# Kernel optimization log

Measured on AMD Instinct MI355X. Metric: run time of the kernel, lower is better.

## Reference

```python
import jax, jax.numpy as jnp
import numpy as np

N, E = 100000, 1000000
IN_F, HID, OUT, K = 64, 64, 32, 3


def setup_inputs() -> dict:
    key = jax.random.key(0)
    ks = jax.random.split(key, 8)
    s = 0.05
    return {
        "features": jax.random.normal(ks[0], (N, IN_F), dtype=jnp.float32),
        "src": jax.random.randint(ks[1], (E,), 0, N),
        "dst": jax.random.randint(ks[2], (E,), 0, N),
        "n_nodes": N,
        "W1": jax.random.normal(ks[3], (K * IN_F, HID), jnp.float32) * s,
        "b1": jnp.zeros((HID,), jnp.float32),
        "W2": jax.random.normal(ks[4], (K * HID, HID), jnp.float32) * s,
        "b2": jnp.zeros((HID,), jnp.float32),
        "Wm1": jax.random.normal(ks[5], (HID, HID), jnp.float32) * s,
        "bm1": jnp.zeros((HID,), jnp.float32),
        "Wm2": jax.random.normal(ks[6], (HID, OUT), jnp.float32) * s,
        "bm2": jnp.zeros((OUT,), jnp.float32),
    }


def _cheb_conv(x, src, dst, dinv, W, b, n_nodes, k=K):
    # DGL ChebConv with lambda_max = 2 (re_norm = 2/lambda_max = 1).
    def prop(h):  # D^{-1/2} A D^{-1/2} h via edge gather/scatter
        m = (h * dinv)[src]                                   # [E, F]
        agg = jax.ops.segment_sum(m, dst, num_segments=n_nodes)
        return agg * dinv

    X0 = x
    Xs = [X0]
    X1 = -prop(X0)                 # -re_norm*L h + (re_norm-1)*X0, re_norm=1
    Xs.append(X1)
    for _ in range(2, k):
        Xi = -2.0 * prop(X1) - X0  # Chebyshev recursion
        Xs.append(Xi)
        X0, X1 = X1, Xi
    return jnp.concatenate(Xs, axis=1) @ W + b  # Linear(k*F_in -> F_out)


def reference(features, src, dst, n_nodes, W1, b1, W2, b2, Wm1, bm1, Wm2, bm2):
    deg = jax.ops.segment_sum(
        jnp.ones((src.shape[0],), dtype=features.dtype), dst, num_segments=n_nodes
    )
    dinv = (jnp.clip(deg, 1.0, None) ** -0.5)[:, None]  # in-degree^{-1/2}
    x = jax.nn.relu(_cheb_conv(features, src, dst, dinv, W1, b1, n_nodes))
    x = jax.nn.relu(_cheb_conv(x, src, dst, dinv, W2, b2, n_nodes))
    return jax.nn.relu(x @ Wm1 + bm1) @ Wm2 + bm2
```

## Files before the change

### kernel.cpp

```cpp
#include <hip/hip_runtime.h>


typedef unsigned short ushort_t;
typedef __attribute__((ext_vector_type(8))) short v8s;
typedef __attribute__((ext_vector_type(4))) float v4f;

__device__ inline ushort_t f2bf(float f) {
    unsigned u = __float_as_uint(f);
    return (ushort_t)((u + 0x7FFFu + ((u >> 16) & 1u)) >> 16);
}
__device__ inline float bf2f(ushort_t h) {
    return __uint_as_float(((unsigned)h) << 16);
}

#define BSH 9
#define BSZ (1 << BSH)
#define CHUNK 4096

__global__ void k_wprep(const float* __restrict__ W1, const float* __restrict__ W2,
                        const float* __restrict__ Wm1, const float* __restrict__ Wm2,
                        ushort_t* __restrict__ W1t, ushort_t* __restrict__ W2t,
                        ushort_t* __restrict__ Wm1t, ushort_t* __restrict__ Wm2t,
                        int* __restrict__ gbase, int* __restrict__ done, int NB) {
    int i = blockIdx.x * 256 + threadIdx.x;
    if (i < 12288) { int k = i >> 6, n = i & 63; W1t[n * 192 + k] = f2bf(W1[i]); return; }
    i -= 12288;
    if (i < 12288) { int k = i >> 6, n = i & 63; W2t[n * 192 + k] = f2bf(W2[i]); return; }
    i -= 12288;
    if (i < 4096) { int k = i >> 6, n = i & 63; Wm1t[n * 64 + k] = f2bf(Wm1[i]); return; }
    i -= 4096;
    if (i < 2048) { int k = i >> 5, n = i & 31; Wm2t[n * 64 + k] = f2bf(Wm2[i]); return; }
    i -= 2048;
    if (i < NB) gbase[i] = 0;
    if (i == NB) *done = 0;
}

__global__ __launch_bounds__(256) void k_bhist(const int* __restrict__ dst,
                                               int* __restrict__ gbase,
                                               int* __restrict__ gcur,
                                               int* __restrict__ done, int E, int NB) {
    __shared__ int h[1024];
    __shared__ int isLast;
    for (int i = threadIdx.x; i < NB; i += 256) h[i] = 0;
    __syncthreads();
    for (int i = blockIdx.x * blockDim.x + threadIdx.x; i < E; i += gridDim.x * blockDim.x)
        atomicAdd(&h[dst[i] >> BSH], 1);
    __syncthreads();
    for (int i = threadIdx.x; i < NB; i += 256)
        if (h[i]) atomicAdd(&gbase[i], h[i]);
    __threadfence();
    __syncthreads();
    if (threadIdx.x == 0) isLast = (atomicAdd(done, 1) == (int)gridDim.x - 1);
    __syncthreads();
    if (isLast) {
        __threadfence();
        int t = threadIdx.x;
        int v = (t < NB) ? gbase[t] : 0;
        h[t] = v;
        __syncthreads();
        for (int off = 1; off < 256; off <<= 1) {
            int u = (t >= off) ? h[t - off] : 0;
            __syncthreads();
            h[t] += u;
            __syncthreads();
        }
        if (t < NB) {
            int excl = h[t] - v;
            gbase[t] = excl;
            gcur[t] = excl;
        }
    }
}

__global__ __launch_bounds__(256) void k_bucket2(
    const int* __restrict__ src, const int* __restrict__ dst,
    int* __restrict__ gcur, int2* __restrict__ eb, int E, int NB) {
    __shared__ int ls[CHUNK];
    __shared__ int ld[CHUNK];
    __shared__ int hist[1024];
    __shared__ int bbase[1024];
    int t = threadIdx.x;
    int base = blockIdx.x * CHUNK;
    int count = E - base;
    if (count > CHUNK) count = CHUNK;
    for (int i = t; i < NB; i += 256) hist[i] = 0;
    __syncthreads();
    for (int i = t; i < count; i += 256) {
        int s = src[base + i];
        int d = dst[base + i];
        ls[i] = s;
        ld[i] = d;
        atomicAdd(&hist[d >> BSH], 1);
    }
    __syncthreads();
    for (int b = t; b < NB; b += 256) {
        int c = hist[b];
        bbase[b] = c ? atomicAdd(&gcur[b], c) : 0;
        hist[b] = 0;
    }
    __syncthreads();
    for (int i = t; i < count; i += 256) {
        int d = ld[i];
        int b = d >> BSH;
        int off = atomicAdd(&hist[b], 1);
        eb[bbase[b] + off] = make_int2(ls[i], d);
    }
}

__global__ __launch_bounds__(256) void k_local(
    const int2* __restrict__ eb, const int* __restrict__ gbase,
    int* __restrict__ col, int* __restrict__ row_ptr,
    float* __restrict__ dinv, int N, int E, int NB) {
    __shared__ int cnt[BSZ];
    __shared__ int tsum[256];
    int t = threadIdx.x;
    int b = blockIdx.x;
    int d0 = b << BSH;
    cnt[2 * t] = 0;
    cnt[2 * t + 1] = 0;
    __syncthreads();
    int beg = gbase[b];
    int end = (b + 1 < NB) ? gbase[b + 1] : E;
    for (int i = beg + t; i < end; i += 256)
        atomicAdd(&cnt[eb[i].y - d0], 1);
    __syncthreads();
    int c0 = cnt[2 * t], c1 = cnt[2 * t + 1];
    int mysum = c0 + c1;
    tsum[t] = mysum;
    __syncthreads();
    for (int off = 1; off < 256; off <<= 1) {
        int u = 0;
        if (t >= off) u = tsum[t - off];
        __syncthreads();
        tsum[t] += u;
        __syncthreads();
    }
    int rbase = beg + tsum[t] - mysum;
    int d = d0 + 2 * t;
    if (d < N) {
        row_ptr[d] = rbase;
        dinv[d] = rsqrtf(fmaxf((float)c0, 1.0f));
    }
    if (d + 1 < N) {
        row_ptr[d + 1] = rbase + c0;
        dinv[d + 1] = rsqrtf(fmaxf((float)c1, 1.0f));
    }
    cnt[2 * t] = rbase;
    cnt[2 * t + 1] = rbase + c0;
    __syncthreads();
    for (int i = beg + t; i < end; i += 256) {
        int2 e = eb[i];
        int p = atomicAdd(&cnt[e.y - d0], 1);
        col[p] = e.x;
    }
    if (b == NB - 1 && t == 0) row_ptr[N] = E;
}

__global__ void k_tobf16(const float4* __restrict__ X, const float* __restrict__ dinv,
                         ushort4* __restrict__ Y, int n4) {
    int i = blockIdx.x * blockDim.x + threadIdx.x;
    if (i < n4) {
        float s = dinv[i >> 4];
        float4 v = X[i];
        ushort4 o;
        o.x = f2bf(v.x * s); o.y = f2bf(v.y * s); o.z = f2bf(v.z * s); o.w = f2bf(v.w * s);
        Y[i] = o;
    }
}

template <int MODE>
__global__ __launch_bounds__(256) void k_prop(
    const ushort_t* __restrict__ Xb, const int* __restrict__ rp,
    const int* __restrict__ col, const float* __restrict__ dinv,
    const ushort_t* __restrict__ X0b, ushort_t* __restrict__ OUTB, int N) {
    int wid = (blockIdx.x * blockDim.x + threadIdx.x) >> 6;
    int lane = threadIdx.x & 63;
    if (wid >= N) return;
    int g = lane >> 4;
    int fl = (lane & 15) * 4;
    int beg = rp[wid], end = rp[wid + 1];
    float4 a0 = make_float4(0.f, 0.f, 0.f, 0.f);
    float4 a1 = make_float4(0.f, 0.f, 0.f, 0.f);
    int e = beg + g;
    for (; e + 4 < end; e += 8) {
        int s0 = col[e], s1 = col[e + 4];
        ushort4 u0 = *(const ushort4*)&Xb[(size_t)s0 * 64 + fl];
        ushort4 u1 = *(const ushort4*)&Xb[(size_t)s1 * 64 + fl];
        a0.x += bf2f(u0.x); a0.y += bf2f(u0.y); a0.z += bf2f(u0.z); a0.w += bf2f(u0.w);
        a1.x += bf2f(u1.x); a1.y += bf2f(u1.y); a1.z += bf2f(u1.z); a1.w += bf2f(u1.w);
    }
    if (e < end) {
        int s0 = col[e];
        ushort4 u0 = *(const ushort4*)&Xb[(size_t)s0 * 64 + fl];
        a0.x += bf2f(u0.x); a0.y += bf2f(u0.y); a0.z += bf2f(u0.z); a0.w += bf2f(u0.w);
    }
    float4 acc;
    acc.x = a0.x + a1.x;
    acc.y = a0.y + a1.y;
    acc.z = a0.z + a1.z;
    acc.w = a0.w + a1.w;
    acc.x += __shfl_xor(acc.x, 16);
    acc.y += __shfl_xor(acc.y, 16);
    acc.z += __shfl_xor(acc.z, 16);
    acc.w += __shfl_xor(acc.w, 16);
    acc.x += __shfl_xor(acc.x, 32);
    acc.y += __shfl_xor(acc.y, 32);
    acc.z += __shfl_xor(acc.z, 32);
    acc.w += __shfl_xor(acc.w, 32);
    if (g == 0) {
        float di = dinv[wid];
        ushort4 ob;
        if (MODE == 1) {
            float m = -di * di;
            ob.x = f2bf(m * acc.x);
            ob.y = f2bf(m * acc.y);
            ob.z = f2bf(m * acc.z);
            ob.w = f2bf(m * acc.w);
        } else {
            ushort4 x0u = *(const ushort4*)&X0b[(size_t)wid * 64 + fl];
            float m = -2.0f * di;
            float rd = 1.0f / di;
            ob.x = f2bf(fmaf(m, acc.x, -rd * bf2f(x0u.x)));
            ob.y = f2bf(fmaf(m, acc.y, -rd * bf2f(x0u.y)));
            ob.z = f2bf(fmaf(m, acc.z, -rd * bf2f(x0u.z)));
            ob.w = f2bf(fmaf(m, acc.w, -rd * bf2f(x0u.w)));
        }
        *(ushort4*)&OUTB[(size_t)wid * 64 + fl] = ob;
    }
}

template <bool SCALE_OUT>
__global__ __launch_bounds__(256, 4) void k_cheb_mfma(
    const ushort_t* __restrict__ X0, const ushort_t* __restrict__ X1,
    const ushort_t* __restrict__ X2, const float* __restrict__ dinv,
    const ushort_t* __restrict__ Wt, const float* __restrict__ b,
    ushort_t* __restrict__ Yb, int N) {
    __shared__ ushort_t XA[3][64][72];
    int tid = threadIdx.x;
    int node0 = blockIdx.x * 64;
    const ushort_t* Xc[3] = {X0, X1, X2};
#pragma unroll
    for (int c = 0; c < 3; c++) {
#pragma unroll
        for (int p = 0; p < 2; p++) {
            int s = p * 2048 + tid * 8;
            int row = s >> 6, cc = s & 63;
            v8s v = *(const v8s*)&Xc[c][((size_t)(node0 + row)) * 64 + cc];
            *(v8s*)&XA[c][row][cc] = v;
        }
    }
    __syncthreads();

    int wave = tid >> 6, lane = tid & 63;
    int n16 = lane & 15, q = lane >> 4;
    int lrow = wave * 16 + n16;
    v8s av[6];
#pragma unroll
    for (int ks = 0; ks < 6; ks++)
        av[ks] = *(const v8s*)&XA[ks >> 1][lrow][(ks & 1) * 32 + q * 8];

    v4f acc_s[4], acc_u[4];
#pragma unroll
    for (int t = 0; t < 4; t++) {
        acc_s[t] = (v4f){0.f, 0.f, 0.f, 0.f};
        acc_u[t] = (v4f){0.f, 0.f, 0.f, 0.f};
    }
#pragma unroll
    for (int ks = 0; ks < 6; ks++) {
        int c = ks >> 1;
#pragma unroll
        for (int t = 0; t < 4; t++) {
            v8s bv = *(const v8s*)&Wt[(size_t)(t * 16 + n16) * 192 + ks * 32 + q * 8];
            if (c < 2)
                acc_s[t] = __builtin_amdgcn_mfma_f32_16x16x32_bf16(av[ks], bv, acc_s[t], 0, 0, 0);
            else
                acc_u[t] = __builtin_amdgcn_mfma_f32_16x16x32_bf16(av[ks], bv, acc_u[t], 0, 0, 0);
        }
    }
    int rbase = node0 + wave * 16 + q * 4;
#pragma unroll
    for (int r = 0; r < 4; r++) {
        int row = rbase + r;
        if (row < N) {
            float dv = dinv[row];
            float rd = 1.0f / dv;
            float s = SCALE_OUT ? dv : 1.0f;
#pragma unroll
            for (int t = 0; t < 4; t++) {
                float y = fmaf(rd, acc_s[t][r], acc_u[t][r]) + b[t * 16 + n16];
                y = fmaxf(y, 0.0f);
                Yb[(size_t)row * 64 + t * 16 + n16] = f2bf(s * y);
            }
        }
    }
}

__global__ __launch_bounds__(256, 4) void k_cheb_mlp(
    const ushort_t* __restrict__ X0, const ushort_t* __restrict__ X1,
    const ushort_t* __restrict__ X2, const float* __restrict__ dinv,
    const ushort_t* __restrict__ Wt, const float* __restrict__ b,
    const ushort_t* __restrict__ Wm1t, const float* __restrict__ bm1,
    const ushort_t* __restrict__ Wm2t, const float* __restrict__ bm2,
    float* __restrict__ out, int N) {
    __shared__ ushort_t smem[3 * 64 * 72];
    ushort_t (*XA)[64][72] = (ushort_t(*)[64][72])smem;
    ushort_t (*Hs0)[76] = (ushort_t(*)[76])smem;
    ushort_t (*Hs1)[76] = (ushort_t(*)[76])(smem + 64 * 76);
    int tid = threadIdx.x;
    int node0 = blockIdx.x * 64;
    const ushort_t* Xc[3] = {X0, X1, X2};
#pragma unroll
    for (int c = 0; c < 3; c++) {
#pragma unroll
        for (int p = 0; p < 2; p++) {
            int s = p * 2048 + tid * 8;
            int row = s >> 6, cc = s & 63;
            v8s v = *(const v8s*)&Xc[c][((size_t)(node0 + row)) * 64 + cc];
            *(v8s*)&XA[c][row][cc] = v;
        }
    }
    __syncthreads();

    int wave = tid >> 6, lane = tid & 63;
    int n16 = lane & 15, q = lane >> 4;
    int lrow = wave * 16 + n16;
    v8s av[6];
#pragma unroll
    for (int ks = 0; ks < 6; ks++)
        av[ks] = *(const v8s*)&XA[ks >> 1][lrow][(ks & 1) * 32 + q * 8];
    __syncthreads();

    v4f acc_s[4], acc_u[4];
#pragma unroll
    for (int t = 0; t < 4; t++) {
        acc_s[t] = (v4f){0.f, 0.f, 0.f, 0.f};
        acc_u[t] = (v4f){0.f, 0.f, 0.f, 0.f};
    }
#pragma unroll
    for (int ks = 0; ks < 6; ks++) {
        int c = ks >> 1;
#pragma unroll
        for (int t = 0; t < 4; t++) {
            v8s bv = *(const v8s*)&Wt[(size_t)(t * 16 + n16) * 192 + ks * 32 + q * 8];
            if (c < 2)
                acc_s[t] = __builtin_amdgcn_mfma_f32_16x16x32_bf16(av[ks], bv, acc_s[t], 0, 0, 0);
            else
                acc_u[t] = __builtin_amdgcn_mfma_f32_16x16x32_bf16(av[ks], bv, acc_u[t], 0, 0, 0);
        }
    }
    int lr = wave * 16 + q * 4;
    int rbase = node0 + lr;
#pragma unroll
    for (int r = 0; r < 4; r++) {
        int row = rbase + r;
        if (row < N) {
            float dv = dinv[row];
            float rd = 1.0f / dv;
#pragma unroll
            for (int t = 0; t < 4; t++) {
                float y = fmaf(rd, acc_s[t][r], acc_u[t][r]) + b[t * 16 + n16];
                Hs0[lr + r][t * 16 + n16] = f2bf(fmaxf(y, 0.0f));
            }
        } else {
#pragma unroll
            for (int t = 0; t < 4; t++) Hs0[lr + r][t * 16 + n16] = 0;
        }
    }
    __syncthreads();

    v4f acc[4];
#pragma unroll
    for (int t = 0; t < 4; t++) acc[t] = (v4f){0.f, 0.f, 0.f, 0.f};
#pragma unroll
    for (int ks = 0; ks < 2; ks++) {
        v8s av1 = *(const v8s*)&Hs0[wave * 16 + n16][ks * 32 + q * 8];
#pragma unroll
        for (int t = 0; t < 4; t++) {
            v8s bv = *(const v8s*)&Wm1t[(size_t)(t * 16 + n16) * 64 + ks * 32 + q * 8];
            acc[t] = __builtin_amdgcn_mfma_f32_16x16x32_bf16(av1, bv, acc[t], 0, 0, 0);
        }
    }
#pragma unroll
    for (int r = 0; r < 4; r++)
#pragma unroll
        for (int t = 0; t < 4; t++) {
            float y = acc[t][r] + bm1[t * 16 + n16];
            Hs1[lr + r][t * 16 + n16] = f2bf(fmaxf(y, 0.0f));
        }
    __syncthreads();

    v4f a2[2];
    a2[0] = (v4f){0.f, 0.f, 0.f, 0.f};
    a2[1] = (v4f){0.f, 0.f, 0.f, 0.f};
#pragma unroll
    for (int ks = 0; ks < 2; ks++) {
        v8s av2 = *(const v8s*)&Hs1[wave * 16 + n16][ks * 32 + q * 8];
#pragma unroll
        for (int t = 0; t < 2; t++) {
            v8s bv = *(const v8s*)&Wm2t[(size_t)(t * 16 + n16) * 64 + ks * 32 + q * 8];
            a2[t] = __builtin_amdgcn_mfma_f32_16x16x32_bf16(av2, bv, a2[t], 0, 0, 0);
        }
    }
#pragma unroll
    for (int r = 0; r < 4; r++) {
        int row = rbase + r;
        if (row < N) {
#pragma unroll
            for (int t = 0; t < 2; t++)
                out[(size_t)row * 32 + t * 16 + n16] = a2[t][r] + bm2[t * 16 + n16];
        }
    }
}

extern "C" void kernel_launch(void* const* d_in, const int* in_sizes, int n_in,
                              void* d_out, int out_size, void* d_ws, size_t ws_size,
                              hipStream_t stream) {
    const float* features = (const float*)d_in[0];
    const int* src = (const int*)d_in[1];
    const int* dst = (const int*)d_in[2];
    const float* W1 = (const float*)d_in[4];
    const float* b1 = (const float*)d_in[5];
    const float* W2 = (const float*)d_in[6];
    const float* b2 = (const float*)d_in[7];
    const float* Wm1 = (const float*)d_in[8];
    const float* bm1 = (const float*)d_in[9];
    const float* Wm2 = (const float*)d_in[10];
    const float* bm2 = (const float*)d_in[11];
    float* out = (float*)d_out;

    int N = in_sizes[0] / 64;
    int E = in_sizes[1];
    int NB = (N + BSZ - 1) >> BSH;

    float* ws = (float*)d_ws;
    float* dinv = ws;
    int* row_ptr = (int*)(dinv + N);
    int* gbase = row_ptr + (N + 1);
    int* gcur = gbase + 1024;
    int* done = gcur + 1024;
    int* col = done + 16;
    int2* eb = (int2*)(((uintptr_t)(col + E) + 7) & ~(uintptr_t)7);
    ushort_t* Fb  = (ushort_t*)(eb + E);
    ushort_t* X1b = Fb  + (size_t)N * 64;
    ushort_t* X2b = X1b + (size_t)N * 64;
    ushort_t* H1b = X2b + (size_t)N * 64;
    ushort_t* W1t = H1b + (size_t)N * 64;
    ushort_t* W2t = W1t + 64 * 192;
    ushort_t* Wm1t = W2t + 64 * 192;
    ushort_t* Wm2t = Wm1t + 64 * 64;

    int pblk = (N * 64 + 255) / 256;
    int gblk = (N + 63) / 64;
    int n4 = N * 16;
    int cblk = (n4 + 255) / 256;
    int bblk = (E + CHUNK - 1) / CHUNK;

    k_wprep<<<(30720 + 1024 + 255) / 256, 256, 0, stream>>>(
        W1, W2, Wm1, Wm2, W1t, W2t, Wm1t, Wm2t, gbase, done, NB);

    k_bhist<<<512, 256, 0, stream>>>(dst, gbase, gcur, done, E, NB);
    k_bucket2<<<bblk, 256, 0, stream>>>(src, dst, gcur, eb, E, NB);
    k_local<<<NB, 256, 0, stream>>>(eb, gbase, col, row_ptr, dinv, N, E, NB);

    k_tobf16<<<cblk, 256, 0, stream>>>((const float4*)features, dinv, (ushort4*)Fb, n4);

    k_prop<1><<<pblk, 256, 0, stream>>>(Fb, row_ptr, col, dinv, nullptr, X1b, N);
    k_prop<2><<<pblk, 256, 0, stream>>>(X1b, row_ptr, col, dinv, Fb, X2b, N);
    k_cheb_mfma<true><<<gblk, 256, 0, stream>>>(Fb, X1b, X2b, dinv, W1t, b1, H1b, N);

    k_prop<1><<<pblk, 256, 0, stream>>>(H1b, row_ptr, col, dinv, nullptr, X1b, N);
    k_prop<2><<<pblk, 256, 0, stream>>>(X1b, row_ptr, col, dinv, H1b, X2b, N);
    k_cheb_mlp<<<gblk, 256, 0, stream>>>(H1b, X1b, X2b, dinv, W2t, b2,
                                         Wm1t, bm1, Wm2t, bm2, out, N);
}
```

Before: 402.5 us.

## Fuse second Chebyshev propagation into the MFMA linear kernels

```diff
diff --git a/kernel.cpp b/kernel.cpp
--- a/kernel.cpp
+++ b/kernel.cpp
@@ -166,6 +166,34 @@
         o.x = f2bf(v.x * s); o.y = f2bf(v.y * s); o.z = f2bf(v.z * s); o.w = f2bf(v.w * s);
         Y[i] = o;
     }
+}
+
+__device__ inline float4 gather_sum(const ushort_t* __restrict__ Xb,
+                                    const int* __restrict__ col,
+                                    int beg, int end, int g, int fl) {
+    float4 a0 = make_float4(0.f, 0.f, 0.f, 0.f);
+    float4 a1 = make_float4(0.f, 0.f, 0.f, 0.f);
+    int e = beg + g;
+    for (; e + 4 < end; e += 8) {
+        int s0 = col[e], s1 = col[e + 4];
+        ushort4 u0 = *(const ushort4*)&Xb[(size_t)s0 * 64 + fl];
+        ushort4 u1 = *(const ushort4*)&Xb[(size_t)s1 * 64 + fl];
+        a0.x += bf2f(u0.x); a0.y += bf2f(u0.y); a0.z += bf2f(u0.z); a0.w += bf2f(u0.w);
+        a1.x += bf2f(u1.x); a1.y += bf2f(u1.y); a1.z += bf2f(u1.z); a1.w += bf2f(u1.w);
+    }
+    if (e < end) {
+        int s0 = col[e];
+        ushort4 u0 = *(const ushort4*)&Xb[(size_t)s0 * 64 + fl];
+        a0.x += bf2f(u0.x); a0.y += bf2f(u0.y); a0.z += bf2f(u0.z); a0.w += bf2f(u0.w);
+    }
+    float4 acc;
+    acc.x = a0.x + a1.x; acc.y = a0.y + a1.y;
+    acc.z = a0.z + a1.z; acc.w = a0.w + a1.w;
+    acc.x += __shfl_xor(acc.x, 16); acc.y += __shfl_xor(acc.y, 16);
+    acc.z += __shfl_xor(acc.z, 16); acc.w += __shfl_xor(acc.w, 16);
+    acc.x += __shfl_xor(acc.x, 32); acc.y += __shfl_xor(acc.y, 32);
+    acc.z += __shfl_xor(acc.z, 32); acc.w += __shfl_xor(acc.w, 32);
+    return acc;
 }
 
 template <int MODE>
@@ -229,126 +257,160 @@
     }
 }
 
-template <bool SCALE_OUT>
-__global__ __launch_bounds__(256, 4) void k_cheb_mfma(
-    const ushort_t* __restrict__ X0, const ushort_t* __restrict__ X1,
-    const ushort_t* __restrict__ X2, const float* __restrict__ dinv,
-    const ushort_t* __restrict__ Wt, const float* __restrict__ b,
-    ushort_t* __restrict__ Yb, int N) {
-    __shared__ ushort_t XA[3][64][72];
+__global__ __launch_bounds__(512, 8) void k_pc1(
+    const ushort_t* __restrict__ Xb, const int* __restrict__ rp,
+    const int* __restrict__ col, const float* __restrict__ dinv,
+    const ushort_t* __restrict__ T0, const ushort_t* __restrict__ Wt,
+    const float* __restrict__ b, ushort_t* __restrict__ Yb, int N) {
+    __shared__ ushort_t XA[64][72];
     int tid = threadIdx.x;
+    int w = tid >> 6, lane = tid & 63;
+    int g = lane >> 4, fl = (lane & 15) * 4;
     int node0 = blockIdx.x * 64;
-    const ushort_t* Xc[3] = {X0, X1, X2};
-#pragma unroll
-    for (int c = 0; c < 3; c++) {
-#pragma unroll
-        for (int p = 0; p < 2; p++) {
-            int s = p * 2048 + tid * 8;
-            int row = s >> 6, cc = s & 63;
-            v8s v = *(const v8s*)&Xc[c][((size_t)(node0 + row)) * 64 + cc];
-            *(v8s*)&XA[c][row][cc] = v;
-        }
-    }
-    __syncthreads();
-
-    int wave = tid >> 6, lane = tid & 63;
+
+    for (int i = 0; i < 8; i++) {
+        int nd = node0 + w * 8 + i;
+        ushort4 ob;
+        ob.x = 0; ob.y = 0; ob.z = 0; ob.w = 0;
+        if (nd < N) {
+            float4 acc = gather_sum(Xb, col, rp[nd], rp[nd + 1], g, fl);
+            if (g == 0) {
+                float di = dinv[nd];
+                ushort4 x0u = *(const ushort4*)&T0[(size_t)nd * 64 + fl];
+                float m = -2.0f * di;
+                float rd = 1.0f / di;
+                ob.x = f2bf(fmaf(m, acc.x, -rd * bf2f(x0u.x)));
+                ob.y = f2bf(fmaf(m, acc.y, -rd * bf2f(x0u.y)));
+                ob.z = f2bf(fmaf(m, acc.z, -rd * bf2f(x0u.z)));
+                ob.w = f2bf(fmaf(m, acc.w, -rd * bf2f(x0u.w)));
+            }
+        }
+        if (g == 0) *(ushort4*)&XA[w * 8 + i][fl] = ob;
+    }
+    __syncthreads();
+
     int n16 = lane & 15, q = lane >> 4;
-    int lrow = wave * 16 + n16;
-    v8s av[6];
-#pragma unroll
-    for (int ks = 0; ks < 6; ks++)
-        av[ks] = *(const v8s*)&XA[ks >> 1][lrow][(ks & 1) * 32 + q * 8];
-
-    v4f acc_s[4], acc_u[4];
-#pragma unroll
-    for (int t = 0; t < 4; t++) {
-        acc_s[t] = (v4f){0.f, 0.f, 0.f, 0.f};
-        acc_u[t] = (v4f){0.f, 0.f, 0.f, 0.f};
-    }
+    int f = w >> 1, h = w & 1;
+    int arow = node0 + f * 16 + n16;
+
+    v4f acc_s[2], acc_u[2];
+    acc_s[0] = (v4f){0.f, 0.f, 0.f, 0.f};
+    acc_s[1] = (v4f){0.f, 0.f, 0.f, 0.f};
+    acc_u[0] = (v4f){0.f, 0.f, 0.f, 0.f};
+    acc_u[1] = (v4f){0.f, 0.f, 0.f, 0.f};
 #pragma unroll
     for (int ks = 0; ks < 6; ks++) {
         int c = ks >> 1;
-#pragma unroll
-        for (int t = 0; t < 4; t++) {
+        int kk = (ks & 1) * 32 + q * 8;
+        v8s av = {0, 0, 0, 0, 0, 0, 0, 0};
+        if (c == 2) {
+            av = *(const v8s*)&XA[f * 16 + n16][kk];
+        } else {
+            const ushort_t* P = (c == 0) ? T0 : Xb;
+            if (arow < N) av = *(const v8s*)&P[(size_t)arow * 64 + kk];
+        }
+#pragma unroll
+        for (int t2 = 0; t2 < 2; t2++) {
+            int t = h * 2 + t2;
             v8s bv = *(const v8s*)&Wt[(size_t)(t * 16 + n16) * 192 + ks * 32 + q * 8];
             if (c < 2)
-                acc_s[t] = __builtin_amdgcn_mfma_f32_16x16x32_bf16(av[ks], bv, acc_s[t], 0, 0, 0);
+                acc_s[t2] = __builtin_amdgcn_mfma_f32_16x16x32_bf16(av, bv, acc_s[t2], 0, 0, 0);
             else
-                acc_u[t] = __builtin_amdgcn_mfma_f32_16x16x32_bf16(av[ks], bv, acc_u[t], 0, 0, 0);
-        }
-    }
-    int rbase = node0 + wave * 16 + q * 4;
+                acc_u[t2] = __builtin_amdgcn_mfma_f32_16x16x32_bf16(av, bv, acc_u[t2], 0, 0, 0);
+        }
+    }
+    int rbase = node0 + f * 16 + q * 4;
 #pragma unroll
     for (int r = 0; r < 4; r++) {
         int row = rbase + r;
         if (row < N) {
             float dv = dinv[row];
             float rd = 1.0f / dv;
-            float s = SCALE_OUT ? dv : 1.0f;
-#pragma unroll
-            for (int t = 0; t < 4; t++) {
-                float y = fmaf(rd, acc_s[t][r], acc_u[t][r]) + b[t * 16 + n16];
+#pragma unroll
+            for (int t2 = 0; t2 < 2; t2++) {
+                int t = h * 2 + t2;
+                float y = fmaf(rd, acc_s[t2][r], acc_u[t2][r]) + b[t * 16 + n16];
                 y = fmaxf(y, 0.0f);
-                Yb[(size_t)row * 64 + t * 16 + n16] = f2bf(s * y);
+                Yb[(size_t)row * 64 + t * 16 + n16] = f2bf(dv * y);
             }
         }
     }
 }
 
-__global__ __launch_bounds__(256, 4) void k_cheb_mlp(
-    const ushort_t* __restrict__ X0, const ushort_t* __restrict__ X1,
-    const ushort_t* __restrict__ X2, const float* __restrict__ dinv,
-    const ushort_t* __restrict__ Wt, const float* __restrict__ b,
+__global__ __launch_bounds__(512, 8) void k_pc2(
+    const ushort_t* __restrict__ Xb, const int* __restrict__ rp,
+    const int* __restrict__ col, const float* __restrict__ dinv,
+    const ushort_t* __restrict__ T0, const ushort_t* __restrict__ Wt,
+    const float* __restrict__ b,
     const ushort_t* __restrict__ Wm1t, const float* __restrict__ bm1,
     const ushort_t* __restrict__ Wm2t, const float* __restrict__ bm2,
     float* __restrict__ out, int N) {
-    __shared__ ushort_t smem[3 * 64 * 72];
-    ushort_t (*XA)[64][72] = (ushort_t(*)[64][72])smem;
+    __shared__ ushort_t smem[9728];
+    ushort_t (*XA)[72] = (ushort_t(*)[72])smem;
     ushort_t (*Hs0)[76] = (ushort_t(*)[76])smem;
     ushort_t (*Hs1)[76] = (ushort_t(*)[76])(smem + 64 * 76);
     int tid = threadIdx.x;
+    int w = tid >> 6, lane = tid & 63;
+    int g = lane >> 4, fl = (lane & 15) * 4;
     int node0 = blockIdx.x * 64;
-    const ushort_t* Xc[3] = {X0, X1, X2};
-#pragma unroll
-    for (int c = 0; c < 3; c++) {
-#pragma unroll
-        for (int p = 0; p < 2; p++) {
-            int s = p * 2048 + tid * 8;
-            int row = s >> 6, cc = s & 63;
-            v8s v = *(const v8s*)&Xc[c][((size_t)(node0 + row)) * 64 + cc];
-            *(v8s*)&XA[c][row][cc] = v;
-        }
-    }
-    __syncthreads();
-
-    int wave = tid >> 6, lane = tid & 63;
+
+    for (int i = 0; i < 8; i++) {
+        int nd = node0 + w * 8 + i;
+        ushort4 ob;
+        ob.x = 0; ob.y = 0; ob.z = 0; ob.w = 0;
+        if (nd < N) {
+            float4 acc = gather_sum(Xb, col, rp[nd], rp[nd + 1], g, fl);
+            if (g == 0) {
+                float di = dinv[nd];
+                ushort4 x0u = *(const ushort4*)&T0[(size_t)nd * 64 + fl];
+                float m = -2.0f * di;
+                float rd = 1.0f / di;
+                ob.x = f2bf(fmaf(m, acc.x, -rd * bf2f(x0u.x)));
+                ob.y = f2bf(fmaf(m, acc.y, -rd * bf2f(x0u.y)));
+                ob.z = f2bf(fmaf(m, acc.z, -rd * bf2f(x0u.z)));
+                ob.w = f2bf(fmaf(m, acc.w, -rd * bf2f(x0u.w)));
+            }
+        }
+        if (g == 0) *(ushort4*)&XA[w * 8 + i][fl] = ob;
+    }
+    __syncthreads();
+
     int n16 = lane & 15, q = lane >> 4;
-    int lrow = wave * 16 + n16;
-    v8s av[6];
-#pragma unroll
-    for (int ks = 0; ks < 6; ks++)
-        av[ks] = *(const v8s*)&XA[ks >> 1][lrow][(ks & 1) * 32 + q * 8];
-    __syncthreads();
-
-    v4f acc_s[4], acc_u[4];
-#pragma unroll
-    for (int t = 0; t < 4; t++) {
-        acc_s[t] = (v4f){0.f, 0.f, 0.f, 0.f};
-        acc_u[t] = (v4f){0.f, 0.f, 0.f, 0.f};
-    }
+    int f = w >> 1, h = w & 1;
+    int arow = node0 + f * 16 + n16;
+
+    v8s av4 = *(const v8s*)&XA[f * 16 + n16][q * 8];
+    v8s av5 = *(const v8s*)&XA[f * 16 + n16][32 + q * 8];
+    __syncthreads();
+
+    v4f acc_s[2], acc_u[2];
+    acc_s[0] = (v4f){0.f, 0.f, 0.f, 0.f};
+    acc_s[1] = (v4f){0.f, 0.f, 0.f, 0.f};
+    acc_u[0] = (v4f){0.f, 0.f, 0.f, 0.f};
+    acc_u[1] = (v4f){0.f, 0.f, 0.f, 0.f};
 #pragma unroll
     for (int ks = 0; ks < 6; ks++) {
         int c = ks >> 1;
-#pragma unroll
-        for (int t = 0; t < 4; t++) {
+        int kk = (ks & 1) * 32 + q * 8;
+        v8s av;
+        if (c == 2) {
+            av = (ks & 1) ? av5 : av4;
+        } else {
+            const ushort_t* P = (c == 0) ? T0 : Xb;
+            av = (v8s){0, 0, 0, 0, 0, 0, 0, 0};
+            if (arow < N) av = *(const v8s*)&P[(size_t)arow * 64 + kk];
+        }
+#pragma unroll
+        for (int t2 = 0; t2 < 2; t2++) {
+            int t = h * 2 + t2;
             v8s bv = *(const v8s*)&Wt[(size_t)(t * 16 + n16) * 192 + ks * 32 + q * 8];
             if (c < 2)
-                acc_s[t] = __builtin_amdgcn_mfma_f32_16x16x32_bf16(av[ks], bv, acc_s[t], 0, 0, 0);
+                acc_s[t2] = __builtin_amdgcn_mfma_f32_16x16x32_bf16(av, bv, acc_s[t2], 0, 0, 0);
             else
-                acc_u[t] = __builtin_amdgcn_mfma_f32_16x16x32_bf16(av[ks], bv, acc_u[t], 0, 0, 0);
-        }
-    }
-    int lr = wave * 16 + q * 4;
+                acc_u[t2] = __builtin_amdgcn_mfma_f32_16x16x32_bf16(av, bv, acc_u[t2], 0, 0, 0);
+        }
+    }
+    int lr = f * 16 + q * 4;
     int rbase = node0 + lr;
 #pragma unroll
     for (int r = 0; r < 4; r++) {
@@ -357,58 +419,54 @@
             float dv = dinv[row];
             float rd = 1.0f / dv;
 #pragma unroll
-            for (int t = 0; t < 4; t++) {
-                float y = fmaf(rd, acc_s[t][r], acc_u[t][r]) + b[t * 16 + n16];
+            for (int t2 = 0; t2 < 2; t2++) {
+                int t = h * 2 + t2;
+                float y = fmaf(rd, acc_s[t2][r], acc_u[t2][r]) + b[t * 16 + n16];
                 Hs0[lr + r][t * 16 + n16] = f2bf(fmaxf(y, 0.0f));
             }
         } else {
 #pragma unroll
-            for (int t = 0; t < 4; t++) Hs0[lr + r][t * 16 + n16] = 0;
-        }
-    }
-    __syncthreads();
-
-    v4f acc[4];
-#pragma unroll
-    for (int t = 0; t < 4; t++) acc[t] = (v4f){0.f, 0.f, 0.f, 0.f};
+            for (int t2 = 0; t2 < 2; t2++)
+                Hs0[lr + r][(h * 2 + t2) * 16 + n16] = 0;
+        }
+    }
+    __syncthreads();
+
+    v4f acc[2];
+    acc[0] = (v4f){0.f, 0.f, 0.f, 0.f};
+    acc[1] = (v4f){0.f, 0.f, 0.f, 0.f};
 #pragma unroll
     for (int ks = 0; ks < 2; ks++) {
-        v8s av1 = *(const v8s*)&Hs0[wave * 16 + n16][ks * 32 + q * 8];
-#pragma unroll
-        for (int t = 0; t < 4; t++) {
+        v8s av1 = *(const v8s*)&Hs0[f * 16 + n16][ks * 32 + q * 8];
+#pragma unroll
+        for (int t2 = 0; t2 < 2; t2++) {
+            int t = h * 2 + t2;
             v8s bv = *(const v8s*)&Wm1t[(size_t)(t * 16 + n16) * 64 + ks * 32 + q * 8];
-            acc[t] = __builtin_amdgcn_mfma_f32_16x16x32_bf16(av1, bv, acc[t], 0, 0, 0);
+            acc[t2] = __builtin_amdgcn_mfma_f32_16x16x32_bf16(av1, bv, acc[t2], 0, 0, 0);
         }
     }
 #pragma unroll
     for (int r = 0; r < 4; r++)
 #pragma unroll
-        for (int t = 0; t < 4; t++) {
-            float y = acc[t][r] + bm1[t * 16 + n16];
+        for (int t2 = 0; t2 < 2; t2++) {
+            int t = h * 2 + t2;
+            float y = acc[t2][r] + bm1[t * 16 + n16];
             Hs1[lr + r][t * 16 + n16] = f2bf(fmaxf(y, 0.0f));
         }
     __syncthreads();
 
-    v4f a2[2];
-    a2[0] = (v4f){0.f, 0.f, 0.f, 0.f};
-    a2[1] = (v4f){0.f, 0.f, 0.f, 0.f};
+    v4f a2 = (v4f){0.f, 0.f, 0.f, 0.f};
 #pragma unroll
     for (int ks = 0; ks < 2; ks++) {
-        v8s av2 = *(const v8s*)&Hs1[wave * 16 + n16][ks * 32 + q * 8];
-#pragma unroll
-        for (int t = 0; t < 2; t++) {
-            v8s bv = *(const v8s*)&Wm2t[(size_t)(t * 16 + n16) * 64 + ks * 32 + q * 8];
-            a2[t] = __builtin_amdgcn_mfma_f32_16x16x32_bf16(av2, bv, a2[t], 0, 0, 0);
-        }
+        v8s av2 = *(const v8s*)&Hs1[f * 16 + n16][ks * 32 + q * 8];
+        v8s bv = *(const v8s*)&Wm2t[(size_t)(h * 16 + n16) * 64 + ks * 32 + q * 8];
+        a2 = __builtin_amdgcn_mfma_f32_16x16x32_bf16(av2, bv, a2, 0, 0, 0);
     }
 #pragma unroll
     for (int r = 0; r < 4; r++) {
         int row = rbase + r;
-        if (row < N) {
-#pragma unroll
-            for (int t = 0; t < 2; t++)
-                out[(size_t)row * 32 + t * 16 + n16] = a2[t][r] + bm2[t * 16 + n16];
-        }
+        if (row < N)
+            out[(size_t)row * 32 + h * 16 + n16] = a2[r] + bm2[h * 16 + n16];
     }
 }
 
@@ -442,8 +500,7 @@
     int2* eb = (int2*)(((uintptr_t)(col + E) + 7) & ~(uintptr_t)7);
     ushort_t* Fb  = (ushort_t*)(eb + E);
     ushort_t* X1b = Fb  + (size_t)N * 64;
-    ushort_t* X2b = X1b + (size_t)N * 64;
-    ushort_t* H1b = X2b + (size_t)N * 64;
+    ushort_t* H1b = X1b + (size_t)N * 64;
     ushort_t* W1t = H1b + (size_t)N * 64;
     ushort_t* W2t = W1t + 64 * 192;
     ushort_t* Wm1t = W2t + 64 * 192;
@@ -465,11 +522,9 @@
     k_tobf16<<<cblk, 256, 0, stream>>>((const float4*)features, dinv, (ushort4*)Fb, n4);
 
     k_prop<1><<<pblk, 256, 0, stream>>>(Fb, row_ptr, col, dinv, nullptr, X1b, N);
-    k_prop<2><<<pblk, 256, 0, stream>>>(X1b, row_ptr, col, dinv, Fb, X2b, N);
-    k_cheb_mfma<true><<<gblk, 256, 0, stream>>>(Fb, X1b, X2b, dinv, W1t, b1, H1b, N);
+    k_pc1<<<gblk, 512, 0, stream>>>(X1b, row_ptr, col, dinv, Fb, W1t, b1, H1b, N);
 
     k_prop<1><<<pblk, 256, 0, stream>>>(H1b, row_ptr, col, dinv, nullptr, X1b, N);
-    k_prop<2><<<pblk, 256, 0, stream>>>(X1b, row_ptr, col, dinv, H1b, X2b, N);
-    k_cheb_mlp<<<gblk, 256, 0, stream>>>(H1b, X1b, X2b, dinv, W2t, b2,
-                                         Wm1t, bm1, Wm2t, bm2, out, N);
-}
+    k_pc2<<<gblk, 512, 0, stream>>>(X1b, row_ptr, col, dinv, H1b, W2t, b2,
+                                    Wm1t, bm1, Wm2t, bm2, out, N);
+}
```

New measurement: 398.9 us. Within noise of the previous version (-0.9%).
